# Optimization experiments

Hardware: AMD Instinct MI355X
Metric: run time of the kernel (lower is better)

The kernel has to match this reference:

```python
import jax, jax.numpy as jnp
import numpy as np

N_U, N_I, D = 30000, 15000, 64
L = 2                 # propagation layers (self.l)
TEMP = 0.2
LAMBDA1, LAMBDA2 = 0.2, 1e-7
H, F = 4, 16          # GAT heads x per-head dim; H*F == D
NEG_SLOPE = 0.2
AVG_DEG = 16
B = 2048


def setup_inputs() -> dict:
    key = jax.random.key(0)
    ks = jax.random.split(key, 10)
    rng = np.random.default_rng(0)
    E_u_0 = jax.random.normal(ks[0], (N_U, D), jnp.float32) * 0.1
    E_i_0 = jax.random.normal(ks[1], (N_I, D), jnp.float32) * 0.1
    # sparse normalized bipartite adjacency (adj_norm) as an edge list
    nnz = N_U * AVG_DEG
    u_idx = np.repeat(np.arange(N_U), AVG_DEG)
    i_idx = rng.integers(0, N_I, nnz)
    deg_u = np.bincount(u_idx, minlength=N_U)
    deg_i = np.maximum(np.bincount(i_idx, minlength=N_I), 1)
    vals = (1.0 / np.sqrt(deg_u[u_idx] * deg_i[i_idx])).astype(np.float32)
    # GAT graph on n_u+n_i nodes: bipartite edges both directions + self-loops
    n = N_U + N_I
    src = np.concatenate([u_idx, i_idx + N_U, np.arange(n)]).astype(np.int32)
    dst = np.concatenate([i_idx + N_U, u_idx, np.arange(n)]).astype(np.int32)
    # GAT parameters (fresh each forward in original, so just random)
    W = jax.random.normal(ks[2], (D, H * F), jnp.float32) / np.sqrt(D)
    attn_l = jax.random.normal(ks[3], (H, F), jnp.float32) * 0.1
    attn_r = jax.random.normal(ks[4], (H, F), jnp.float32) * 0.1
    uids = jax.random.randint(ks[5], (B,), 0, N_U, jnp.int32)
    iids = jax.random.randint(ks[6], (B,), 0, N_I, jnp.int32)
    pos = jax.random.randint(ks[7], (B,), 0, N_I, jnp.int32)
    neg = jax.random.randint(ks[8], (B,), 0, N_I, jnp.int32)
    return dict(E_u_0=E_u_0, E_i_0=E_i_0, adj_vals=jnp.asarray(vals),
                W=W, attn_l=attn_l, attn_r=attn_r,
                u_idx=jnp.asarray(u_idx, jnp.int32), i_idx=jnp.asarray(i_idx, jnp.int32),
                src=jnp.asarray(src), dst=jnp.asarray(dst),
                uids=uids, iids=iids, pos=pos, neg=neg)


def gat_layer(h, src, dst, W, attn_l, attn_r, n_nodes):
    # GATConv: project, per-edge attention, neighborhood softmax, scatter-agg
    feat = (h @ W).reshape(-1, H, F)                      # [N,H,F]
    el = (feat * attn_l).sum(-1)                          # [N,H]
    er = (feat * attn_r).sum(-1)                          # [N,H]
    e = jax.nn.leaky_relu(el[src] + er[dst], NEG_SLOPE)   # [E,H]
    e_max = jax.ops.segment_max(e, dst, num_segments=n_nodes)
    a = jnp.exp(e - e_max[dst])
    denom = jax.ops.segment_sum(a, dst, num_segments=n_nodes)
    a = a / denom[dst]                                    # self-loops => denom>0
    out = jax.ops.segment_sum(a[:, :, None] * feat[src], dst, num_segments=n_nodes)
    return jax.nn.elu(out.reshape(-1, H * F))             # [N,D]


def _forward(E_u_0, E_i_0, adj_vals, W, attn_l, attn_r,
             u_idx, i_idx, src, dst, uids, iids, pos, neg):
    n = N_U + N_I
    Eu, Ei = E_u_0, E_i_0
    sum_Eu, sum_Ei = E_u_0, E_i_0
    sum_Gu, sum_Gi = E_u_0, E_i_0
    for _ in range(L):
        # LightGCN spmm propagation: Z_u = A @ E_i, Z_i = A.T @ E_u
        Zu = jax.ops.segment_sum(adj_vals[:, None] * Ei[i_idx], u_idx, num_segments=N_U)
        Zi = jax.ops.segment_sum(adj_vals[:, None] * Eu[u_idx], i_idx, num_segments=N_I)
        ls1 = gat_layer(jnp.concatenate([Eu, Ei], 0), src, dst, W, attn_l, attn_r, n)
        Gu, Gi = ls1[:N_U], ls1[N_U:]
        Eu, Ei = Zu + Eu, Zi + Ei
        sum_Eu = sum_Eu + Eu
        sum_Ei = sum_Ei + Ei
        sum_Gu = sum_Gu + Gu
        sum_Gi = sum_Gi + Gi
    log_eps = jnp.float32(np.log(1e-8))
    # InfoNCE: log(sum(exp(s)) + 1e-8) == logaddexp(logsumexp(s), log(1e-8))
    lse_u = jax.scipy.special.logsumexp(sum_Gu[uids] @ sum_Eu.T / TEMP, axis=1)
    lse_i = jax.scipy.special.logsumexp(sum_Gi[iids] @ sum_Ei.T / TEMP, axis=1)
    neg_score = jnp.logaddexp(lse_u, log_eps).mean() + jnp.logaddexp(lse_i, log_eps).mean()
    pos_score = ((sum_Gu[uids] * sum_Eu[uids]).sum(1) / TEMP).mean() \
              + ((sum_Gi[iids] * sum_Ei[iids]).sum(1) / TEMP).mean()
    loss_s = -pos_score + neg_score
    # BPR loss
    u_emb = sum_Eu[uids]
    diff = (u_emb * sum_Ei[pos]).sum(-1) - (u_emb * sum_Ei[neg]).sum(-1)
    loss_r = -jax.nn.log_sigmoid(diff).mean()
    # L2 reg over nn.Parameters (E_u_0, E_i_0 only)
    loss_reg = LAMBDA2 * ((E_u_0 ** 2).sum() + (E_i_0 ** 2).sum())
    loss = loss_r + LAMBDA1 * loss_s + loss_reg
    return loss, loss_r, LAMBDA1 * loss_s


def reference(E_u_0, E_i_0, adj_vals, W, attn_l, attn_r,
              u_idx, i_idx, src, dst, uids, iids, pos, neg):
    return _forward(E_u_0, E_i_0, adj_vals, W, attn_l, attn_r,
                    u_idx, i_idx, src, dst, uids, iids, pos, neg)
```

## Files before the change

kernel.cpp:

```cpp
#include <hip/hip_runtime.h>
#include <math.h>

#define N_U 30000
#define N_I 15000
#define N_TOT 45000
#define D 64
#define NNZ 480000
#define B 2048
#define INV_TEMP 5.0f
#define LOG_EPS -18.420680743952367f
#define NEG_SLOPE 0.2f
#define LAMBDA1 0.2f
#define LAMBDA2 1e-7f

#define NSP 128
#define RSP_U 235
#define RSP_I 118
#define PAD_U 30016
#define PAD_I 15040
#define SCALE_LOG2 7.2134752044448170f
#define LN2F 0.6931471805599453f

typedef __attribute__((ext_vector_type(8))) short short8;
typedef __attribute__((ext_vector_type(4))) float f32x4;

__device__ inline float wred(float v) {
#pragma unroll
  for (int o = 32; o > 0; o >>= 1) v += __shfl_down(v, o, 64);
  return v;
}

__device__ inline float leaky(float v) { return (v >= 0.f) ? v : NEG_SLOPE * v; }

__device__ inline void atomMaxF(float* a, float v) {
  if (v >= 0.f) atomicMax((int*)a, __float_as_int(v));
  else atomicMin((unsigned int*)a, __float_as_uint(v));
}

__device__ inline unsigned short f2bf(float x) {
  unsigned u = __float_as_uint(x);
  unsigned r = u + 0x7FFFu + ((u >> 16) & 1u);
  return (unsigned short)(r >> 16);
}
__device__ inline float bf2f(unsigned short h) {
  return __uint_as_float(((unsigned)h) << 16);
}

__global__ void k_init(const float* __restrict__ Eu0, const float* __restrict__ Ei0,
                       float* fU, float* fI,
                       unsigned short* gU, unsigned short* gI,
                       float* sEu, float* sEi,
                       float* sGu, float* sGi, int* deg, float* acc) {
  int t = blockIdx.x * 256 + threadIdx.x;
  if (t < 20) acc[t] = (t >= 8 && t < 16) ? -INFINITY : 0.f;
  if (t < N_I) deg[t] = 0;
  if (t < N_U * D) {
    int n = t >> 6, c = t & 63;
    float v = Eu0[t];
    fU[(size_t)n * 128 + c] = v;
    gU[(size_t)n * 128 + c] = f2bf(v);
    sEu[t] = v; sGu[t] = v;
  } else if (t < N_TOT * D) {
    int j = t - N_U * D;
    int n = j >> 6, c = j & 63;
    float v = Ei0[j];
    fI[(size_t)n * 128 + c] = v;
    gI[(size_t)n * 128 + c] = f2bf(v);
    sEi[j] = v; sGi[j] = v;
  }
}

__global__ void k_deg(const int* __restrict__ ii, int* deg) {
  int e = blockIdx.x * 256 + threadIdx.x;
  if (e < NNZ) atomicAdd(&deg[ii[e]], 1);
}

__global__ void k_scan(const int* __restrict__ deg, int* rowptr, int* cursor) {
  __shared__ int tsum[1024];
  const int CHUNK = 15;
  int tid = threadIdx.x;
  int base = tid * CHUNK;
  int s = 0;
#pragma unroll
  for (int k = 0; k < CHUNK; k++) {
    int idx = base + k;
    s += (idx < N_I) ? deg[idx] : 0;
  }
  tsum[tid] = s;
  __syncthreads();
  for (int o = 1; o < 1024; o <<= 1) {
    int x = (tid >= o) ? tsum[tid - o] : 0;
    __syncthreads();
    tsum[tid] += x;
    __syncthreads();
  }
  int excl = tsum[tid] - s;
#pragma unroll
  for (int k = 0; k < CHUNK; k++) {
    int idx = base + k;
    if (idx < N_I) {
      rowptr[idx] = excl;
      cursor[idx] = excl;
      excl += deg[idx];
    }
  }
  if (tid == 1023) rowptr[N_I] = tsum[1023];
}

__global__ void k_fill(const int* __restrict__ ii, const float* __restrict__ vals,
                       int* cursor, int* u_srt, float* v_srt) {
  int e = blockIdx.x * 256 + threadIdx.x;
  if (e < NNZ) {
    int pos = atomicAdd(&cursor[ii[e]], 1);
    u_srt[pos] = e >> 4;
    v_srt[pos] = vals[e];
  }
}

__global__ void k_feat(float* __restrict__ fU, float* __restrict__ fI,
                       unsigned short* __restrict__ gU, unsigned short* __restrict__ gI,
                       const float* __restrict__ W, const float* __restrict__ al,
                       const float* __restrict__ ar,
                       float* __restrict__ el, float* __restrict__ er,
                       float* __restrict__ elmx) {
  __shared__ float Ws[64 * 64];
  __shared__ float hs[16][64];
  __shared__ float bmax[4];
  int tid = threadIdx.x;
  if (tid < 4) bmax[tid] = -INFINITY;
  for (int t = tid; t < 1024; t += 256) ((float4*)Ws)[t] = ((const float4*)W)[t];
  int g = tid >> 6, c = tid & 63;
  int n0 = blockIdx.x * 16 + g * 4;
  float* rows[4];
  unsigned short* grows[4];
#pragma unroll
  for (int j = 0; j < 4; j++) {
    int node = n0 + j;
    rows[j] = nullptr; grows[j] = nullptr;
    if (node < N_TOT) {
      if (node < N_U) {
        rows[j] = fU + (size_t)node * 128;
        grows[j] = gU + (size_t)node * 128;
      } else {
        rows[j] = fI + (size_t)(node - N_U) * 128;
        grows[j] = gI + (size_t)(node - N_U) * 128;
      }
      hs[g * 4 + j][c] = rows[j][c];
    }
  }
  __syncthreads();
  float a0 = 0.f, a1 = 0.f, a2 = 0.f, a3 = 0.f;
#pragma unroll 8
  for (int k = 0; k < 64; ++k) {
    float w = Ws[k * 64 + c];
    a0 = fmaf(hs[g * 4 + 0][k], w, a0);
    a1 = fmaf(hs[g * 4 + 1][k], w, a1);
    a2 = fmaf(hs[g * 4 + 2][k], w, a2);
    a3 = fmaf(hs[g * 4 + 3][k], w, a3);
  }
  float accs[4] = {a0, a1, a2, a3};
  float alc = al[c], arc = ar[c];
  float lmx = -INFINITY;
#pragma unroll
  for (int j = 0; j < 4; j++) {
    int node = n0 + j;
    if (node >= N_TOT) continue;
    rows[j][64 + c] = accs[j];
    grows[j][64 + c] = f2bf(accs[j]);
    float pl = accs[j] * alc;
    float pr = accs[j] * arc;
#pragma unroll
    for (int o = 8; o >= 1; o >>= 1) {
      pl += __shfl_down(pl, o, 16);
      pr += __shfl_down(pr, o, 16);
    }
    if ((c & 15) == 0) {
      el[node * 4 + (c >> 4)] = pl;
      er[node * 4 + (c >> 4)] = pr;
      lmx = fmaxf(lmx, pl);
    }
  }
  if ((c & 15) == 0) {
    int h2 = c >> 4;
    if (lmx >= 0.f) atomicMax((int*)&bmax[h2], __float_as_int(lmx));
    else atomicMin((unsigned int*)&bmax[h2], __float_as_uint(lmx));
  }
  __syncthreads();
  if (tid < 4) atomMaxF(elmx + tid, bmax[tid]);
}

__global__ void k_layer(const float* __restrict__ fU_cur, const float* __restrict__ fI_cur,
                        const unsigned short* __restrict__ gU_cur,
                        const unsigned short* __restrict__ gI_cur,
                        const float* __restrict__ el, const float* __restrict__ er,
                        const float* __restrict__ vals, const int* __restrict__ ii,
                        const int* __restrict__ rowptr, const int* __restrict__ u_srt,
                        const float* __restrict__ v_srt,
                        const float* __restrict__ elmx,
                        float* __restrict__ fU_nxt, float* __restrict__ fI_nxt,
                        unsigned short* __restrict__ gU_nxt, unsigned short* __restrict__ gI_nxt,
                        float* __restrict__ sEu, float* __restrict__ sEi,
                        float* __restrict__ sGu, float* __restrict__ sGi,
                        unsigned short* __restrict__ EuH, unsigned short* __restrict__ EuL,
                        unsigned short* __restrict__ EiH, unsigned short* __restrict__ EiL,
                        float* __restrict__ normU, float* __restrict__ normI) {
  int t = blockIdx.x * 256 + threadIdx.x;
  int node = t >> 6, c = t & 63;
  if (node >= N_TOT) return;
  int h = c >> 4;

  if (node < N_U) {
    int u = node;
    float eru = er[u * 4 + h];
    float m = leaky(elmx[h] + eru);
    const float* selfrow = fU_cur + (size_t)u * 128;
    float aself = __expf(leaky(el[u * 4 + h] + eru) - m);

    int idx[16]; float vv[16];
#pragma unroll
    for (int k = 0; k < 16; k++) { idx[k] = ii[u * 16 + k]; vv[k] = vals[u * 16 + k]; }
    float av[16];
#pragma unroll
    for (int k = 0; k < 16; k++)
      av[k] = __expf(leaky(el[(idx[k] + N_U) * 4 + h] + eru) - m);

    float den = aself;
#pragma unroll
    for (int k = 0; k < 16; k++) den += av[k];

    float o0 = aself * selfrow[64 + c], o1 = 0.f;
    float z0 = 0.f, z1 = 0.f;
#pragma unroll
    for (int k = 0; k < 16; k += 2) {
      const unsigned short* rA = gI_cur + (size_t)idx[k] * 128;
      const unsigned short* rB = gI_cur + (size_t)idx[k + 1] * 128;
      float eA = bf2f(rA[c]), fA = bf2f(rA[64 + c]);
      float eB = bf2f(rB[c]), fB = bf2f(rB[64 + c]);
      z0 = fmaf(vv[k], eA, z0);
      z1 = fmaf(vv[k + 1], eB, z1);
      o0 = fmaf(av[k], fA, o0);
      o1 = fmaf(av[k + 1], fB, o1);
    }
    float o = (o0 + o1) / den;
    float g = (o > 0.f) ? o : expm1f(o);
    float e_new = selfrow[c] + z0 + z1;
    fU_nxt[(size_t)u * 128 + c] = e_new;
    gU_nxt[(size_t)u * 128 + c] = f2bf(e_new);
    size_t off = (size_t)u * D + c;
    float s_final = sEu[off] + e_new;
    sEu[off] = s_final;
    sGu[off] += g;
    if (EuH) {
      unsigned short hi = f2bf(s_final);
      EuH[off] = hi;
      EuL[off] = f2bf(s_final - bf2f(hi));
      float n2 = wred(s_final * s_final);
      if (c == 0) normU[u] = n2;
    }
  } else {
    int i = node - N_U;
    float eri = er[node * 4 + h];
    float m = leaky(elmx[h] + eri);
    const float* selfrow = fI_cur + (size_t)i * 128;
    float aself = __expf(leaky(el[node * 4 + h] + eri) - m);
    float den0 = aself, den1 = 0.f;
    float o0 = aself * selfrow[64 + c], o1 = 0.f;
    float z0 = 0.f, z1 = 0.f;
    int r0 = rowptr[i], r1 = rowptr[i + 1];
    int r = r0;
    for (; r + 3 < r1; r += 4) {
      int u0 = u_srt[r], u1 = u_srt[r + 1], u2 = u_srt[r + 2], u3 = u_srt[r + 3];
      float v0 = v_srt[r], v1 = v_srt[r + 1], v2 = v_srt[r + 2], v3 = v_srt[r + 3];
      float a0 = __expf(leaky(el[u0 * 4 + h] + eri) - m);
      float a1 = __expf(leaky(el[u1 * 4 + h] + eri) - m);
      float a2 = __expf(leaky(el[u2 * 4 + h] + eri) - m);
      float a3 = __expf(leaky(el[u3 * 4 + h] + eri) - m);
      const unsigned short* R0 = gU_cur + (size_t)u0 * 128;
      const unsigned short* R1 = gU_cur + (size_t)u1 * 128;
      const unsigned short* R2 = gU_cur + (size_t)u2 * 128;
      const unsigned short* R3 = gU_cur + (size_t)u3 * 128;
      float e0 = bf2f(R0[c]), f0 = bf2f(R0[64 + c]);
      float e1 = bf2f(R1[c]), f1 = bf2f(R1[64 + c]);
      float e2 = bf2f(R2[c]), f2 = bf2f(R2[64 + c]);
      float e3 = bf2f(R3[c]), f3 = bf2f(R3[64 + c]);
      z0 = fmaf(v0, e0, z0); z1 = fmaf(v1, e1, z1);
      z0 = fmaf(v2, e2, z0); z1 = fmaf(v3, e3, z1);
      den0 += a0 + a2; den1 += a1 + a3;
      o0 = fmaf(a0, f0, o0); o1 = fmaf(a1, f1, o1);
      o0 = fmaf(a2, f2, o0); o1 = fmaf(a3, f3, o1);
    }
    for (; r < r1; r++) {
      int u0 = u_srt[r];
      float v0 = v_srt[r];
      float a0 = __expf(leaky(el[u0 * 4 + h] + eri) - m);
      const unsigned short* R0 = gU_cur + (size_t)u0 * 128;
      float e0 = bf2f(R0[c]), f0 = bf2f(R0[64 + c]);
      z0 = fmaf(v0, e0, z0);
      den0 += a0;
      o0 = fmaf(a0, f0, o0);
    }
    float o = (o0 + o1) / (den0 + den1);
    float g = (o > 0.f) ? o : expm1f(o);
    float e_new = selfrow[c] + z0 + z1;
    fI_nxt[(size_t)i * 128 + c] = e_new;
    gI_nxt[(size_t)i * 128 + c] = f2bf(e_new);
    size_t off = (size_t)i * D + c;
    float s_final = sEi[off] + e_new;
    sEi[off] = s_final;
    sGi[off] += g;
    if (EiH) {
      unsigned short hi = f2bf(s_final);
      EiH[off] = hi;
      EiL[off] = f2bf(s_final - bf2f(hi));
      float n2 = wred(s_final * s_final);
      if (c == 0) normI[i] = n2;
    }
  }
}

__global__ void k_normreg(const float* __restrict__ nU, const float* __restrict__ nI,
                          const float* __restrict__ Eu0, const float* __restrict__ Ei0,
                          float* __restrict__ acc) {
  __shared__ float red[4][3];
  int tid = threadIdx.x;
  int lane = tid & 63, wv = tid >> 6;
  float mu = 0.f, mi = 0.f, s = 0.f;
  for (int t = blockIdx.x * 256 + tid; t < N_U; t += 128 * 256) mu = fmaxf(mu, nU[t]);
  for (int t = blockIdx.x * 256 + tid; t < N_I; t += 128 * 256) mi = fmaxf(mi, nI[t]);
  const float4* A = (const float4*)Eu0;
  const float4* Bp = (const float4*)Ei0;
  const int nA = N_U * 16, nTot = N_TOT * 16;
  for (int t = blockIdx.x * 256 + tid; t < nTot; t += 128 * 256) {
    float4 v = (t < nA) ? A[t] : Bp[t - nA];
    s += v.x * v.x + v.y * v.y + v.z * v.z + v.w * v.w;
  }
#pragma unroll
  for (int o = 32; o > 0; o >>= 1) {
    mu = fmaxf(mu, __shfl_down(mu, o, 64));
    mi = fmaxf(mi, __shfl_down(mi, o, 64));
    s += __shfl_down(s, o, 64);
  }
  if (lane == 0) { red[wv][0] = mu; red[wv][1] = mi; red[wv][2] = s; }
  __syncthreads();
  if (tid == 0) {
    float a = fmaxf(fmaxf(red[0][0], red[1][0]), fmaxf(red[2][0], red[3][0]));
    float b = fmaxf(fmaxf(red[0][1], red[1][1]), fmaxf(red[2][1], red[3][1]));
    float ssum = red[0][2] + red[1][2] + red[2][2] + red[3][2];
    atomMaxF(acc + 6, a);
    atomMaxF(acc + 7, b);
    unsafeAtomicAdd(acc + 5, ssum);
  }
}

__global__ void k_cvt_q(const float* __restrict__ sGu, const float* __restrict__ sGi,
                        const int* __restrict__ uids, const int* __restrict__ iids,
                        unsigned short* __restrict__ QuH, unsigned short* __restrict__ QuL,
                        unsigned short* __restrict__ QiH, unsigned short* __restrict__ QiL,
                        const float* __restrict__ acc,
                        float* __restrict__ M0u, float* __restrict__ M0i) {
  int lane = threadIdx.x & 63, wv = threadIdx.x >> 6;
  int row = blockIdx.x * 4 + wv;
  int side = row >> 11;
  int b = row & (B - 1);
  int id = side ? iids[b] : uids[b];
  float x = (side ? sGi : sGu)[(size_t)id * 64 + lane] * SCALE_LOG2;
  unsigned short hi = f2bf(x);
  unsigned short lo = f2bf(x - bf2f(hi));
  if (side) { QiH[(size_t)b * 64 + lane] = hi; QiL[(size_t)b * 64 + lane] = lo; }
  else      { QuH[(size_t)b * 64 + lane] = hi; QuL[(size_t)b * 64 + lane] = lo; }
  float n2 = wred(x * x);
  if (lane == 0) {
    float en2 = side ? acc[7] : acc[6];
    float M0 = sqrtf(n2) * sqrtf(en2) * 1.01f + 1.0f;
    (side ? M0i : M0u)[b] = M0;
  }
}

__global__ __launch_bounds__(256, 2) void k_lse_mfma(
    const unsigned short* __restrict__ QuH, const unsigned short* __restrict__ QuL,
    const unsigned short* __restrict__ EuHp, const unsigned short* __restrict__ EuLp,
    const unsigned short* __restrict__ QiH, const unsigned short* __restrict__ QiL,
    const unsigned short* __restrict__ EiHp, const unsigned short* __restrict__ EiLp,
    const float* __restrict__ M0u, const float* __restrict__ M0i,
    float* __restrict__ psU, float* __restrict__ psI) {
  int z = blockIdx.z;
  const unsigned short* Qhi = z ? QiH : QuH;
  const unsigned short* Qlo = z ? QiL : QuL;
  const unsigned short* Ehi = z ? EiHp : EuHp;
  const unsigned short* Elo = z ? EiLp : EuLp;
  const float* M0arr = z ? M0i : M0u;
  float* part_s = z ? psI : psU;
  int n_rows = z ? N_I : N_U;
  int rows_per_split = z ? RSP_I : RSP_U;

  int tid = threadIdx.x;
  int wave = tid >> 6, lane = tid & 63;
  int l15 = lane & 15, quad = lane >> 4;
  int qbase = (blockIdx.x * 4 + wave) * 128;
  int split = blockIdx.y;
  int row0 = split * rows_per_split;
  int row_end = min(row0 + rows_per_split, n_rows);
  int rows = row_end - row0; if (rows < 0) rows = 0;
  int total = (rows + 15) >> 4;
  int ntail = rows & 15;

  float ss[8][4];
#pragma unroll
  for (int t = 0; t < 8; t++)
#pragma unroll
    for (int g = 0; g < 4; g++) ss[t][g] = 0.f;

  if (total > 0) {
    short8 ah[8][2], al[8][2];
#pragma unroll
    for (int t = 0; t < 8; t++)
#pragma unroll
      for (int c = 0; c < 2; c++) {
        size_t idx = (size_t)(qbase + t * 16 + l15) * 64 + c * 32 + quad * 8;
        ah[t][c] = *(const short8*)(Qhi + idx);
        al[t][c] = *(const short8*)(Qlo + idx);
      }

    f32x4 cinit[8];
#pragma unroll
    for (int t = 0; t < 8; t++)
#pragma unroll
      for (int g = 0; g < 4; g++)
        cinit[t][g] = -M0arr[qbase + t * 16 + quad * 4 + g];

    const unsigned short* ph = Ehi + (size_t)(row0 + l15) * 64 + quad * 8;
    const unsigned short* pl = Elo + (size_t)(row0 + l15) * 64 + quad * 8;

    short8 cb0 = *(const short8*)(ph);
    short8 cb1 = *(const short8*)(ph + 32);
    short8 cb2 = *(const short8*)(pl);
    short8 cb3 = *(const short8*)(pl + 32);
    ph += 1024; pl += 1024;

    for (int it = 0; it < total - 1; it++) {
      short8 nb0 = *(const short8*)(ph);
      short8 nb1 = *(const short8*)(ph + 32);
      short8 nb2 = *(const short8*)(pl);
      short8 nb3 = *(const short8*)(pl + 32);
      ph += 1024; pl += 1024;
#pragma unroll
      for (int t = 0; t < 8; t++) {
        f32x4 acc = cinit[t];
        acc = __builtin_amdgcn_mfma_f32_16x16x32_bf16(ah[t][0], cb0, acc, 0, 0, 0);
        acc = __builtin_amdgcn_mfma_f32_16x16x32_bf16(ah[t][1], cb1, acc, 0, 0, 0);
        acc = __builtin_amdgcn_mfma_f32_16x16x32_bf16(al[t][0], cb0, acc, 0, 0, 0);
        acc = __builtin_amdgcn_mfma_f32_16x16x32_bf16(al[t][1], cb1, acc, 0, 0, 0);
        acc = __builtin_amdgcn_mfma_f32_16x16x32_bf16(ah[t][0], cb2, acc, 0, 0, 0);
        acc = __builtin_amdgcn_mfma_f32_16x16x32_bf16(ah[t][1], cb3, acc, 0, 0, 0);
#pragma unroll
        for (int g = 0; g < 4; g++)
          ss[t][g] += exp2f(acc[g]);
      }
      cb0 = nb0; cb1 = nb1; cb2 = nb2; cb3 = nb3;
    }
    {
      bool valid = (ntail == 0) || (l15 < ntail);
#pragma unroll
      for (int t = 0; t < 8; t++) {
        f32x4 acc = cinit[t];
        acc = __builtin_amdgcn_mfma_f32_16x16x32_bf16(ah[t][0], cb0, acc, 0, 0, 0);
        acc = __builtin_amdgcn_mfma_f32_16x16x32_bf16(ah[t][1], cb1, acc, 0, 0, 0);
        acc = __builtin_amdgcn_mfma_f32_16x16x32_bf16(al[t][0], cb0, acc, 0, 0, 0);
        acc = __builtin_amdgcn_mfma_f32_16x16x32_bf16(al[t][1], cb1, acc, 0, 0, 0);
        acc = __builtin_amdgcn_mfma_f32_16x16x32_bf16(ah[t][0], cb2, acc, 0, 0, 0);
        acc = __builtin_amdgcn_mfma_f32_16x16x32_bf16(ah[t][1], cb3, acc, 0, 0, 0);
#pragma unroll
        for (int g = 0; g < 4; g++) {
          float e = exp2f(acc[g]);
          ss[t][g] += valid ? e : 0.f;
        }
      }
    }
  }

#pragma unroll
  for (int off = 1; off < 16; off <<= 1) {
#pragma unroll
    for (int t = 0; t < 8; t++)
#pragma unroll
      for (int g = 0; g < 4; g++)
        ss[t][g] += __shfl_xor(ss[t][g], off, 64);
  }

  if (l15 == 0) {
#pragma unroll
    for (int t = 0; t < 8; t++)
#pragma unroll
      for (int g = 0; g < 4; g++) {
        int q = qbase + t * 16 + quad * 4 + g;
        part_s[(size_t)split * B + q] = ss[t][g];
      }
  }
}

__global__ void k_small(const float* __restrict__ sEu, const float* __restrict__ sEi,
                        const float* __restrict__ sGu, const float* __restrict__ sGi,
                        const int* __restrict__ uids, const int* __restrict__ iids,
                        const int* __restrict__ pos, const int* __restrict__ neg,
                        const float* __restrict__ psU, const float* __restrict__ psI,
                        const float* __restrict__ M0u, const float* __restrict__ M0i,
                        float* acc, float* __restrict__ out) {
  int b = blockIdx.x * 256 + threadIdx.x;
  float du = 0.f, di = 0.f, nu = 0.f, ni = 0.f, bpr = 0.f;
  if (b < B) {
    float su = 0.f, si = 0.f;
    for (int s2 = 0; s2 < NSP; s2++) su += psU[(size_t)s2 * B + b];
    for (int s2 = 0; s2 < NSP; s2++) si += psI[(size_t)s2 * B + b];
    float lseu = M0u[b] * LN2F + logf(su);
    float lsei = M0i[b] * LN2F + logf(si);
    nu = fmaxf(lseu, LOG_EPS) + log1pf(expf(-fabsf(lseu - LOG_EPS)));
    ni = fmaxf(lsei, LOG_EPS) + log1pf(expf(-fabsf(lsei - LOG_EPS)));

    int u = uids[b], it = iids[b], p = pos[b], ng = neg[b];
    const float4* gu = (const float4*)(sGu + (size_t)u * D);
    const float4* eu = (const float4*)(sEu + (size_t)u * D);
    const float4* gi = (const float4*)(sGi + (size_t)it * D);
    const float4* ei = (const float4*)(sEi + (size_t)it * D);
    const float4* ep = (const float4*)(sEi + (size_t)p * D);
    const float4* en = (const float4*)(sEi + (size_t)ng * D);
    float diff = 0.f;
#pragma unroll
    for (int k = 0; k < 16; k++) {
      float4 a = gu[k], b4 = eu[k];
      du += a.x * b4.x + a.y * b4.y + a.z * b4.z + a.w * b4.w;
      float4 c = gi[k], d4 = ei[k];
      di += c.x * d4.x + c.y * d4.y + c.z * d4.z + c.w * d4.w;
      float4 e = ep[k], f = en[k];
      diff += b4.x * (e.x - f.x) + b4.y * (e.y - f.y) + b4.z * (e.z - f.z) + b4.w * (e.w - f.w);
    }
    bpr = (diff > 0.f) ? log1pf(expf(-diff)) : (-diff + log1pf(expf(diff)));
  }
  du = wred(du); di = wred(di); nu = wred(nu); ni = wred(ni); bpr = wred(bpr);
  if ((threadIdx.x & 63) == 0) {
    unsafeAtomicAdd(acc + 0, du);
    unsafeAtomicAdd(acc + 1, di);
    unsafeAtomicAdd(acc + 2, nu);
    unsafeAtomicAdd(acc + 3, ni);
    unsafeAtomicAdd(acc + 4, bpr);
  }
  __syncthreads();
  if (threadIdx.x == 0) {
    __threadfence();
    int ticket = atomicAdd((int*)(acc + 16), 1);
    if (ticket == (int)gridDim.x - 1) {
      __threadfence();
      float a0 = unsafeAtomicAdd(acc + 0, 0.f);
      float a1 = unsafeAtomicAdd(acc + 1, 0.f);
      float a2 = unsafeAtomicAdd(acc + 2, 0.f);
      float a3 = unsafeAtomicAdd(acc + 3, 0.f);
      float a4 = unsafeAtomicAdd(acc + 4, 0.f);
      float a5 = unsafeAtomicAdd(acc + 5, 0.f);
      float pos_score = (a0 + a1) * (INV_TEMP / (float)B);
      float neg_score = (a2 + a3) / (float)B;
      float loss_s = neg_score - pos_score;
      float loss_r = a4 / (float)B;
      float reg = LAMBDA2 * a5;
      out[0] = loss_r + LAMBDA1 * loss_s + reg;
      out[1] = loss_r;
      out[2] = LAMBDA1 * loss_s;
    }
  }
}

extern "C" void kernel_launch(void* const* d_in, const int* in_sizes, int n_in,
                              void* d_out, int out_size, void* d_ws, size_t ws_size,
                              hipStream_t stream) {
  const float* Eu0  = (const float*)d_in[0];
  const float* Ei0  = (const float*)d_in[1];
  const float* vals = (const float*)d_in[2];
  const float* W    = (const float*)d_in[3];
  const float* al   = (const float*)d_in[4];
  const float* ar   = (const float*)d_in[5];
  const int* ii     = (const int*)d_in[7];
  const int* uids   = (const int*)d_in[10];
  const int* iids   = (const int*)d_in[11];
  const int* pos    = (const int*)d_in[12];
  const int* neg    = (const int*)d_in[13];
  float* out = (float*)d_out;

  char* base = (char*)d_ws;
  size_t off = 0;
  auto alloc = [&](size_t bytes) -> void* {
    void* p = base + off;
    off = (off + bytes + 255) & ~(size_t)255;
    return p;
  };
  float* fU_a = (float*)alloc((size_t)N_U * 128 * 4);
  float* fU_b = (float*)alloc((size_t)N_U * 128 * 4);
  float* fI_a = (float*)alloc((size_t)N_I * 128 * 4);
  float* fI_b = (float*)alloc((size_t)N_I * 128 * 4);
  unsigned short* gU_a = (unsigned short*)alloc((size_t)N_U * 128 * 2);
  unsigned short* gU_b = (unsigned short*)alloc((size_t)N_U * 128 * 2);
  unsigned short* gI_a = (unsigned short*)alloc((size_t)N_I * 128 * 2);
  unsigned short* gI_b = (unsigned short*)alloc((size_t)N_I * 128 * 2);
  float* sEu  = (float*)alloc((size_t)N_U * D * 4);
  float* sEi  = (float*)alloc((size_t)N_I * D * 4);
  float* sGu  = (float*)alloc((size_t)N_U * D * 4);
  float* sGi  = (float*)alloc((size_t)N_I * D * 4);
  float* el   = (float*)alloc((size_t)N_TOT * 4 * 4);
  float* er   = (float*)alloc((size_t)N_TOT * 4 * 4);
  float* psU  = (float*)alloc((size_t)B * NSP * 4);
  float* psI  = (float*)alloc((size_t)B * NSP * 4);
  float* M0u  = (float*)alloc((size_t)B * 4);
  float* M0i  = (float*)alloc((size_t)B * 4);
  float* normU= (float*)alloc((size_t)N_U * 4);
  float* normI= (float*)alloc((size_t)N_I * 4);
  float* acc  = (float*)alloc(32 * 4);
  int* deg    = (int*)alloc((size_t)N_I * 4);
  int* cursor = (int*)alloc((size_t)N_I * 4);
  int* rowptr = (int*)alloc((size_t)(N_I + 1) * 4);
  int* u_srt  = (int*)alloc((size_t)NNZ * 4);
  float* v_srt= (float*)alloc((size_t)NNZ * 4);
  unsigned short* EuH = (unsigned short*)alloc((size_t)PAD_U * 64 * 2);
  unsigned short* EuL = (unsigned short*)alloc((size_t)PAD_U * 64 * 2);
  unsigned short* EiH = (unsigned short*)alloc((size_t)PAD_I * 64 * 2);
  unsigned short* EiL = (unsigned short*)alloc((size_t)PAD_I * 64 * 2);
  unsigned short* QuH = (unsigned short*)alloc((size_t)B * 64 * 2);
  unsigned short* QuL = (unsigned short*)alloc((size_t)B * 64 * 2);
  unsigned short* QiH = (unsigned short*)alloc((size_t)B * 64 * 2);
  unsigned short* QiL = (unsigned short*)alloc((size_t)B * 64 * 2);

  k_init<<<(N_TOT * D + 255) / 256, 256, 0, stream>>>(Eu0, Ei0, fU_a, fI_a, gU_a, gI_a,
                                                      sEu, sEi, sGu, sGi, deg, acc);
  k_deg<<<(NNZ + 255) / 256, 256, 0, stream>>>(ii, deg);
  k_scan<<<1, 1024, 0, stream>>>(deg, rowptr, cursor);
  k_fill<<<(NNZ + 255) / 256, 256, 0, stream>>>(ii, vals, cursor, u_srt, v_srt);

  float* cu = fU_a; float* ci = fI_a;
  float* nu = fU_b; float* ni = fI_b;
  unsigned short* gcu = gU_a; unsigned short* gci = gI_a;
  unsigned short* gnu = gU_b; unsigned short* gni = gI_b;
  for (int l = 0; l < 2; ++l) {
    float* elmx = acc + 8 + 4 * l;
    bool last = (l == 1);
    k_feat<<<(N_TOT + 15) / 16, 256, 0, stream>>>(cu, ci, gcu, gci, W, al, ar, el, er, elmx);
    k_layer<<<(N_TOT * D) / 256, 256, 0, stream>>>(
        cu, ci, gcu, gci, el, er, vals, ii, rowptr, u_srt, v_srt, elmx,
        nu, ni, gnu, gni, sEu, sEi, sGu, sGi,
        last ? EuH : nullptr, last ? EuL : nullptr,
        last ? EiH : nullptr, last ? EiL : nullptr,
        normU, normI);
    float* t1 = cu; cu = nu; nu = t1;
    float* t2 = ci; ci = ni; ni = t2;
    unsigned short* t3 = gcu; gcu = gnu; gnu = t3;
    unsigned short* t4 = gci; gci = gni; gni = t4;
  }

  k_normreg<<<128, 256, 0, stream>>>(normU, normI, Eu0, Ei0, acc);
  k_cvt_q<<<(2 * B) / 4, 256, 0, stream>>>(sGu, sGi, uids, iids, QuH, QuL, QiH, QiL, acc, M0u, M0i);
  k_lse_mfma<<<dim3(B / 512, NSP, 2), 256, 0, stream>>>(QuH, QuL, EuH, EuL,
                                                        QiH, QiL, EiH, EiL,
                                                        M0u, M0i, psU, psI);
  k_small<<<B / 256, 256, 0, stream>>>(sEu, sEi, sGu, sGi, uids, iids, pos, neg,
                                       psU, psI, M0u, M0i, acc, out);
}
```

Baseline: 467.9 us.

## Vectorize init copies, warp-shuffle scan, and split el max into separate kernel

The init kernel now processes four floats per thread with float4/ushort4 loads and stores, which cuts thread count and memory transactions. The single-block degree scan replaces its shared-memory Hillis-Steele loop, which had many barriers, with wave-level shuffle scans and keeps the degree values in registers. The per-head max of el is removed from the feature kernel, dropping its shared and global atomics, and is computed in a new small reduction kernel. That adds one extra launch and an extra read of el per layer.

Measured after the change: 424.7 us. -9.2%, faster.

```diff
diff --git a/kernel.cpp b/kernel.cpp
--- a/kernel.cpp
+++ b/kernel.cpp
@@ -54,19 +54,23 @@
   int t = blockIdx.x * 256 + threadIdx.x;
   if (t < 20) acc[t] = (t >= 8 && t < 16) ? -INFINITY : 0.f;
   if (t < N_I) deg[t] = 0;
-  if (t < N_U * D) {
-    int n = t >> 6, c = t & 63;
-    float v = Eu0[t];
-    fU[(size_t)n * 128 + c] = v;
-    gU[(size_t)n * 128 + c] = f2bf(v);
-    sEu[t] = v; sGu[t] = v;
-  } else if (t < N_TOT * D) {
-    int j = t - N_U * D;
-    int n = j >> 6, c = j & 63;
-    float v = Ei0[j];
-    fI[(size_t)n * 128 + c] = v;
-    gI[(size_t)n * 128 + c] = f2bf(v);
-    sEi[j] = v; sGi[j] = v;
+  int n = t >> 4, q = t & 15;
+  if (n < N_U) {
+    float4 v = ((const float4*)Eu0)[t];
+    ((float4*)(fU + (size_t)n * 128))[q] = v;
+    ushort4 bv = {f2bf(v.x), f2bf(v.y), f2bf(v.z), f2bf(v.w)};
+    ((ushort4*)(gU + (size_t)n * 128))[q] = bv;
+    ((float4*)sEu)[t] = v;
+    ((float4*)sGu)[t] = v;
+  } else if (n < N_TOT) {
+    int j = t - N_U * 16;
+    int ni = n - N_U;
+    float4 v = ((const float4*)Ei0)[j];
+    ((float4*)(fI + (size_t)ni * 128))[q] = v;
+    ushort4 bv = {f2bf(v.x), f2bf(v.y), f2bf(v.z), f2bf(v.w)};
+    ((ushort4*)(gI + (size_t)ni * 128))[q] = bv;
+    ((float4*)sEi)[j] = v;
+    ((float4*)sGi)[j] = v;
   }
 }
 
@@ -76,35 +80,48 @@
 }
 
 __global__ void k_scan(const int* __restrict__ deg, int* rowptr, int* cursor) {
-  __shared__ int tsum[1024];
+  __shared__ int wtot[16], woff[16];
   const int CHUNK = 15;
-  int tid = threadIdx.x;
+  int tid = threadIdx.x, lane = tid & 63, wv = tid >> 6;
   int base = tid * CHUNK;
+  int dv[CHUNK];
   int s = 0;
 #pragma unroll
   for (int k = 0; k < CHUNK; k++) {
     int idx = base + k;
-    s += (idx < N_I) ? deg[idx] : 0;
-  }
-  tsum[tid] = s;
+    dv[k] = (idx < N_I) ? deg[idx] : 0;
+    s += dv[k];
+  }
+  int v = s;
+#pragma unroll
+  for (int o = 1; o < 64; o <<= 1) {
+    int x = __shfl_up(v, o, 64);
+    if (lane >= o) v += x;
+  }
+  if (lane == 63) wtot[wv] = v;
   __syncthreads();
-  for (int o = 1; o < 1024; o <<= 1) {
-    int x = (tid >= o) ? tsum[tid - o] : 0;
-    __syncthreads();
-    tsum[tid] += x;
-    __syncthreads();
-  }
-  int excl = tsum[tid] - s;
+  if (tid < 16) {
+    int w = wtot[tid];
+    int iv = w;
+#pragma unroll
+    for (int o = 1; o < 16; o <<= 1) {
+      int x = __shfl_up(iv, o, 16);
+      if (tid >= o) iv += x;
+    }
+    woff[tid] = iv - w;
+  }
+  __syncthreads();
+  int excl = (v - s) + woff[wv];
 #pragma unroll
   for (int k = 0; k < CHUNK; k++) {
     int idx = base + k;
     if (idx < N_I) {
       rowptr[idx] = excl;
       cursor[idx] = excl;
-      excl += deg[idx];
-    }
-  }
-  if (tid == 1023) rowptr[N_I] = tsum[1023];
+      excl += dv[k];
+    }
+  }
+  if (tid == 1023) rowptr[N_I] = excl;
 }
 
 __global__ void k_fill(const int* __restrict__ ii, const float* __restrict__ vals,
@@ -121,13 +138,10 @@
                        unsigned short* __restrict__ gU, unsigned short* __restrict__ gI,
                        const float* __restrict__ W, const float* __restrict__ al,
                        const float* __restrict__ ar,
-                       float* __restrict__ el, float* __restrict__ er,
-                       float* __restrict__ elmx) {
+                       float* __restrict__ el, float* __restrict__ er) {
   __shared__ float Ws[64 * 64];
   __shared__ float hs[16][64];
-  __shared__ float bmax[4];
   int tid = threadIdx.x;
-  if (tid < 4) bmax[tid] = -INFINITY;
   for (int t = tid; t < 1024; t += 256) ((float4*)Ws)[t] = ((const float4*)W)[t];
   int g = tid >> 6, c = tid & 63;
   int n0 = blockIdx.x * 16 + g * 4;
@@ -160,7 +174,6 @@
   }
   float accs[4] = {a0, a1, a2, a3};
   float alc = al[c], arc = ar[c];
-  float lmx = -INFINITY;
 #pragma unroll
   for (int j = 0; j < 4; j++) {
     int node = n0 + j;
@@ -177,16 +190,25 @@
     if ((c & 15) == 0) {
       el[node * 4 + (c >> 4)] = pl;
       er[node * 4 + (c >> 4)] = pr;
-      lmx = fmaxf(lmx, pl);
-    }
-  }
-  if ((c & 15) == 0) {
-    int h2 = c >> 4;
-    if (lmx >= 0.f) atomicMax((int*)&bmax[h2], __float_as_int(lmx));
-    else atomicMin((unsigned int*)&bmax[h2], __float_as_uint(lmx));
-  }
+    }
+  }
+}
+
+__global__ void k_elmax(const float* __restrict__ el, float* __restrict__ dst) {
+  __shared__ float red[4][4];
+  int tid = threadIdx.x;
+  int lane = tid & 63, wv = tid >> 6;
+  float mx = -INFINITY;
+  for (int t = blockIdx.x * 256 + tid; t < N_TOT * 4; t += 64 * 256)
+    mx = fmaxf(mx, el[t]);
+#pragma unroll
+  for (int o = 4; o < 64; o <<= 1) mx = fmaxf(mx, __shfl_xor(mx, o, 64));
+  if (lane < 4) red[wv][lane] = mx;
   __syncthreads();
-  if (tid < 4) atomMaxF(elmx + tid, bmax[tid]);
+  if (tid < 4) {
+    float m2 = fmaxf(fmaxf(red[0][tid], red[1][tid]), fmaxf(red[2][tid], red[3][tid]));
+    atomMaxF(dst + tid, m2);
+  }
 }
 
 __global__ void k_layer(const float* __restrict__ fU_cur, const float* __restrict__ fI_cur,
@@ -625,8 +647,8 @@
   unsigned short* QiH = (unsigned short*)alloc((size_t)B * 64 * 2);
   unsigned short* QiL = (unsigned short*)alloc((size_t)B * 64 * 2);
 
-  k_init<<<(N_TOT * D + 255) / 256, 256, 0, stream>>>(Eu0, Ei0, fU_a, fI_a, gU_a, gI_a,
-                                                      sEu, sEi, sGu, sGi, deg, acc);
+  k_init<<<(N_TOT * 16 + 255) / 256, 256, 0, stream>>>(Eu0, Ei0, fU_a, fI_a, gU_a, gI_a,
+                                                       sEu, sEi, sGu, sGi, deg, acc);
   k_deg<<<(NNZ + 255) / 256, 256, 0, stream>>>(ii, deg);
   k_scan<<<1, 1024, 0, stream>>>(deg, rowptr, cursor);
   k_fill<<<(NNZ + 255) / 256, 256, 0, stream>>>(ii, vals, cursor, u_srt, v_srt);
@@ -638,7 +660,8 @@
   for (int l = 0; l < 2; ++l) {
     float* elmx = acc + 8 + 4 * l;
     bool last = (l == 1);
-    k_feat<<<(N_TOT + 15) / 16, 256, 0, stream>>>(cu, ci, gcu, gci, W, al, ar, el, er, elmx);
+    k_feat<<<(N_TOT + 15) / 16, 256, 0, stream>>>(cu, ci, gcu, gci, W, al, ar, el, er);
+    k_elmax<<<64, 256, 0, stream>>>(el, elmx);
     k_layer<<<(N_TOT * D) / 256, 256, 0, stream>>>(
         cu, ci, gcu, gci, el, er, vals, ii, rowptr, u_srt, v_srt, elmx,
         nu, ni, gnu, gni, sEu, sEi, sGu, sGi,
```
